# Kernel tuning notes

Hardware: AMD Instinct MI355X
Metric: run time of the kernel (lower is better)

Reference implementation:

```python
import jax, jax.numpy as jnp
import numpy as np

NBINS = 256       # kornia equalize_clahe default histogram bins
GRID = (8, 8)     # kornia default grid_size


def _clahe(x, clip_limit):
    """kornia-style CLAHE on x:(C,H,W) in [0,1]; H,W divisible by GRID."""
    C, H, W = x.shape
    GH, GW = GRID
    TH, TW = H // GH, W // GW
    pixels = TH * TW
    # ---- per-tile histograms via flat scatter-add (irregular core) ----
    b_hist = jnp.clip((x * NBINS).astype(jnp.int32), 0, NBINS - 1)  # torch.histc(min=0,max=1) bins
    tiles = b_hist.reshape(C, GH, TH, GW, TW).transpose(0, 1, 3, 2, 4).reshape(-1, pixels)
    ntiles = tiles.shape[0]  # C*GH*GW
    flat = (tiles + (jnp.arange(ntiles, dtype=jnp.int32) * NBINS)[:, None]).ravel()
    hist = jnp.zeros((ntiles * NBINS,), x.dtype).at[flat].add(1.0).reshape(ntiles, NBINS)
    # ---- clip and redistribute excess (kornia _compute_luts) ----
    max_val = jnp.maximum(jnp.floor(clip_limit * pixels / NBINS), 1.0)
    clipped = jnp.minimum(hist, max_val)
    excess = pixels - clipped.sum(-1)                    # (ntiles,), >= 0
    residual = jnp.mod(excess, NBINS)
    redist = (excess - residual) / NBINS
    hist = clipped + redist[:, None] + (jnp.arange(NBINS) < residual[:, None]).astype(x.dtype)
    # ---- LUT from CDF ----
    lut = jnp.floor(jnp.clip(jnp.cumsum(hist, -1) * (NBINS - 1) / pixels, 0, NBINS - 1))
    lut = lut.reshape(C, GH, GW, NBINS)
    # ---- per-pixel bilinear interpolation between 4 neighbouring tile LUTs ----
    def coords(n, T, G):
        g = (jnp.arange(n) + 0.5) / T - 0.5    # fractional tile coordinate
        lo = jnp.clip(jnp.floor(g), 0, G - 1).astype(jnp.int32)
        hi = jnp.clip(lo + 1, 0, G - 1)
        w = jnp.clip(g - jnp.floor(g), 0.0, 1.0).astype(x.dtype)
        return lo, hi, w
    y0, y1, wy = coords(H, TH, GH)
    x0, x1, wx = coords(W, TW, GW)
    b = jnp.clip(jnp.floor(x * (NBINS - 1)).astype(jnp.int32), 0, NBINS - 1)  # lookup bin
    c = jnp.arange(C)[:, None, None]
    def g(ty, tx):  # gather lut[c, ty[h], tx[w], b[c,h,w]] -> (C,H,W)
        return lut[c, ty[None, :, None], tx[None, None, :], b]
    top = g(y0, x0) * (1 - wx)[None, None, :] + g(y0, x1) * wx[None, None, :]
    bot = g(y1, x0) * (1 - wx)[None, None, :] + g(y1, x1) * wx[None, None, :]
    out = top * (1 - wy)[None, :, None] + bot * wy[None, :, None]
    return out / (NBINS - 1)


def _forward(x, log_cor=True):
    shape = x.shape
    mean = x.mean()
    std = jnp.std(x, ddof=1)            # torch .std() is unbiased
    x = (x - mean) / std                # TF.normalize
    xmin, xmax = x.min(), x.max()
    x = (x - xmin) / (xmax - xmin)      # normalize_in_range(x, 0, 1)
    ct_proxy = jnp.std(x, ddof=1)       # x.std([0,1,2]) on 3D input = scalar
    def clahe_branch(xx):
        beta = 10.0 * ct_proxy
        cl = 1.0 / (1.0 - beta) + beta  # data-dependent clip limit
        return _clahe(xx, cl)
    x = jax.lax.cond(ct_proxy < 0.05, clahe_branch, lambda xx: xx, x)
    if log_cor:
        x = jnp.log2(1.0 + x)           # adjust_log with gain=1
    return x.reshape(shape)


def setup_inputs() -> dict:
    key = jax.random.key(0)
    x = jax.random.normal(key, (32, 1024, 1024), dtype=jnp.float32)
    # heavy-tailed distribution -> std/range (ct_proxy) ~ 0.01 < 0.05 so CLAHE branch runs
    x = x ** 3
    return {"x": x}


def reference(x):
    return _forward(x, log_cor=True)
```

## Files before the change

### kernel.cpp

```cpp
#include <hip/hip_runtime.h>
#include <math.h>

#define NC 32
#define NH 1024
#define NW 1024
#define NGH 8
#define NGW 8
#define NTH 128
#define NTW 128
#define NBINS 256
#define NTILES (NC*NGH*NGW)
#define NPIXTOT (NC*NH*NW)
#define TPIX (NTH*NTW)

#define OFF_PSUM   0
#define OFF_PSQ    16384
#define OFF_PMIN   32768
#define OFF_PMAX   40960
#define OFF_PARAMS 49152
#define OFF_HIST   65536
#define OFF_LUT    (OFF_HIST + NTILES*NBINS*4)

__global__ __launch_bounds__(256) void k_reduce(const float* __restrict__ x,
                                                double* __restrict__ ps,
                                                double* __restrict__ ps2,
                                                float* __restrict__ pmn,
                                                float* __restrict__ pmx) {
    int tid = threadIdx.x;
    long g = (long)blockIdx.x * 256 + tid;
    double s = 0.0, s2 = 0.0;
    float mn = INFINITY, mx = -INFINITY;
    const float4* x4 = (const float4*)x;
    const long n4 = NPIXTOT / 4;
    for (long i = g; i < n4; i += (long)2048 * 256) {
        float4 v = x4[i];
        float sf  = (v.x + v.y) + (v.z + v.w);
        float s2f = fmaf(v.x, v.x, fmaf(v.y, v.y, fmaf(v.z, v.z, v.w * v.w)));
        s  += (double)sf;
        s2 += (double)s2f;
        mn = fminf(mn, fminf(fminf(v.x, v.y), fminf(v.z, v.w)));
        mx = fmaxf(mx, fmaxf(fmaxf(v.x, v.y), fmaxf(v.z, v.w)));
    }
    for (int o = 32; o; o >>= 1) {
        s  += __shfl_down(s, o);
        s2 += __shfl_down(s2, o);
        mn = fminf(mn, __shfl_down(mn, o));
        mx = fmaxf(mx, __shfl_down(mx, o));
    }
    __shared__ double shs[4], shs2[4];
    __shared__ float shmn[4], shmx[4];
    int wid = tid >> 6, lane = tid & 63;
    if (lane == 0) { shs[wid] = s; shs2[wid] = s2; shmn[wid] = mn; shmx[wid] = mx; }
    __syncthreads();
    if (tid == 0) {
        double S  = shs[0] + shs[1] + shs[2] + shs[3];
        double S2 = shs2[0] + shs2[1] + shs2[2] + shs2[3];
        float MN = fminf(fminf(shmn[0], shmn[1]), fminf(shmn[2], shmn[3]));
        float MX = fmaxf(fmaxf(shmx[0], shmx[1]), fmaxf(shmx[2], shmx[3]));
        ps[blockIdx.x] = S; ps2[blockIdx.x] = S2; pmn[blockIdx.x] = MN; pmx[blockIdx.x] = MX;
    }
}

__global__ __launch_bounds__(256) void k_params(const double* __restrict__ ps,
                                                const double* __restrict__ ps2,
                                                const float* __restrict__ pmn,
                                                const float* __restrict__ pmx,
                                                float* __restrict__ params) {
    int tid = threadIdx.x;
    double s = 0.0, s2 = 0.0;
    float mn = INFINITY, mx = -INFINITY;
    for (int i = tid; i < 2048; i += 256) {
        s += ps[i]; s2 += ps2[i];
        mn = fminf(mn, pmn[i]); mx = fmaxf(mx, pmx[i]);
    }
    for (int o = 32; o; o >>= 1) {
        s  += __shfl_down(s, o);
        s2 += __shfl_down(s2, o);
        mn = fminf(mn, __shfl_down(mn, o));
        mx = fmaxf(mx, __shfl_down(mx, o));
    }
    __shared__ double shs[4], shs2[4];
    __shared__ float shmn[4], shmx[4];
    int wid = tid >> 6, lane = tid & 63;
    if (lane == 0) { shs[wid] = s; shs2[wid] = s2; shmn[wid] = mn; shmx[wid] = mx; }
    __syncthreads();
    if (tid == 0) {
        double S  = shs[0] + shs[1] + shs[2] + shs[3];
        double S2 = shs2[0] + shs2[1] + shs2[2] + shs2[3];
        float MN = fminf(fminf(shmn[0], shmn[1]), fminf(shmn[2], shmn[3]));
        float MX = fmaxf(fmaxf(shmx[0], shmx[1]), fmaxf(shmx[2], shmx[3]));
        const double n = (double)NPIXTOT;
        double var = (S2 - S * S / n) / (n - 1.0);
        double sd = sqrt(var > 0.0 ? var : 0.0);
        double range = (double)MX - (double)MN;
        double ct = sd / range;
        int flag = (ct < 0.05) ? 1 : 0;
        double beta = 10.0 * ct;
        double cl = 1.0 / (1.0 - beta) + beta;
        double mv = floor(cl * (double)TPIX / (double)NBINS);
        if (mv < 1.0) mv = 1.0;
        params[0] = MN;
        params[1] = (float)(1.0 / range);
        params[2] = (float)mv;
        ((int*)params)[3] = flag;
    }
}

__global__ __launch_bounds__(256) void k_hist(const float* __restrict__ x,
                                              const float* __restrict__ params,
                                              unsigned* __restrict__ hist) {
    __shared__ unsigned lh[NBINS];
    int tid = threadIdx.x;
    int t = blockIdx.x;
    int lane = tid & 63;
    lh[tid] = 0;
    __syncthreads();
    float xmin = params[0], inv = params[1];
    int c = t >> 6, gy = (t >> 3) & 7, gx = t & 7;
    const float* base = x + ((long)c * NH + (long)gy * NTH) * NW + gx * NTW;
    #pragma unroll
    for (int j = 0; j < 16; j++) {
        int l = j * 256 + tid;
        int th = l >> 5, tw4 = l & 31;
        float4 v = *(const float4*)(base + (long)th * NW + tw4 * 4);
        float zv[4] = {v.x, v.y, v.z, v.w};
        #pragma unroll
        for (int k = 0; k < 4; k++) {
            float z = (zv[k] - xmin) * inv;
            int b = (int)(z * 256.0f);
            b = b < 0 ? 0 : (b > 255 ? 255 : b);
            unsigned long long alive = __ballot(1);
            #pragma unroll
            for (int r = 0; r < 3; r++) {
                if (!alive) break;
                int leader = (int)(__ffsll((long long)alive) - 1);
                int lb = __shfl(b, leader);
                unsigned long long m = __ballot(b == lb) & alive;
                if (lane == leader) atomicAdd(&lh[lb], (unsigned)__popcll(m));
                alive &= ~m;
            }
            if ((alive >> lane) & 1ull) atomicAdd(&lh[b], 1u);
        }
    }
    __syncthreads();
    hist[t * NBINS + tid] = lh[tid];
}

__global__ __launch_bounds__(256) void k_lut(const unsigned* __restrict__ hist,
                                             const float* __restrict__ params,
                                             float* __restrict__ lut) {
    int tid = threadIdx.x;
    int t = blockIdx.x;
    int mv = (int)params[2];
    int h = (int)hist[t * NBINS + tid];
    int cl = h < mv ? h : mv;
    __shared__ int sh[NBINS];
    sh[tid] = cl;
    __syncthreads();
    for (int o = 1; o < NBINS; o <<= 1) {
        int v = (tid >= o) ? sh[tid - o] : 0;
        __syncthreads();
        sh[tid] += v;
        __syncthreads();
    }
    int total = sh[NBINS - 1];
    int cdfc = sh[tid];
    int excess = TPIX - total;
    int residual = excess & (NBINS - 1);
    int redist = excess >> 8;
    int cdf = cdfc + redist * (tid + 1) + ((tid + 1) < residual ? (tid + 1) : residual);
    float lv = floorf(fminf((float)cdf * 255.0f / 16384.0f, 255.0f));
    lut[t * NBINS + tid] = lv < 0.0f ? 0.0f : lv;
}

__global__ __launch_bounds__(256) void k_out(const float* __restrict__ x,
                                             const float* __restrict__ params,
                                             const float* __restrict__ lut,
                                             float* __restrict__ out) {
    int tid = threadIdx.x;
    long fid = (long)blockIdx.x * 256 + tid;
    long p = fid * 4;
    int w = (int)(p & (NW - 1));
    int h = (int)((p >> 10) & (NH - 1));
    int c = (int)(p >> 20);
    float xmin = params[0], inv = params[1];
    int flag = ((const int*)params)[3];
    float4 v = *(const float4*)(x + p);
    float gy = (h + 0.5f) * (1.0f / NTH) - 0.5f;
    float fy = floorf(gy);
    float wy = gy - fy;
    int y0 = (int)fy; y0 = y0 < 0 ? 0 : (y0 > 7 ? 7 : y0);
    int y1 = y0 + 1 > 7 ? 7 : y0 + 1;
    const float* lutc = lut + (long)c * 64 * NBINS;
    float zv[4] = {v.x, v.y, v.z, v.w};
    float o4[4];
    #pragma unroll
    for (int k = 0; k < 4; k++) {
        float z = (zv[k] - xmin) * inv;
        float val;
        if (flag) {
            int wk = w + k;
            float gx = (wk + 0.5f) * (1.0f / NTW) - 0.5f;
            float fx = floorf(gx);
            float wx = gx - fx;
            int x0 = (int)fx; x0 = x0 < 0 ? 0 : (x0 > 7 ? 7 : x0);
            int x1 = x0 + 1 > 7 ? 7 : x0 + 1;
            int b = (int)(z * 255.0f);
            b = b < 0 ? 0 : (b > 255 ? 255 : b);
            const float* l00 = lutc + (y0 * 8 + x0) * NBINS;
            const float* l01 = lutc + (y0 * 8 + x1) * NBINS;
            const float* l10 = lutc + (y1 * 8 + x0) * NBINS;
            const float* l11 = lutc + (y1 * 8 + x1) * NBINS;
            float top = l00[b] * (1.0f - wx) + l01[b] * wx;
            float bot = l10[b] * (1.0f - wx) + l11[b] * wx;
            val = (top * (1.0f - wy) + bot * wy) * (1.0f / 255.0f);
        } else {
            val = z;
        }
        o4[k] = log2f(1.0f + val);
    }
    *(float4*)(out + p) = make_float4(o4[0], o4[1], o4[2], o4[3]);
}

extern "C" void kernel_launch(void* const* d_in, const int* in_sizes, int n_in,
                              void* d_out, int out_size, void* d_ws, size_t ws_size,
                              hipStream_t stream) {
    const float* x = (const float*)d_in[0];
    float* out = (float*)d_out;
    char* ws = (char*)d_ws;
    double* ps   = (double*)(ws + OFF_PSUM);
    double* ps2  = (double*)(ws + OFF_PSQ);
    float* pmn   = (float*)(ws + OFF_PMIN);
    float* pmx   = (float*)(ws + OFF_PMAX);
    float* params= (float*)(ws + OFF_PARAMS);
    unsigned* hist = (unsigned*)(ws + OFF_HIST);
    float* lut   = (float*)(ws + OFF_LUT);

    k_reduce<<<2048, 256, 0, stream>>>(x, ps, ps2, pmn, pmx);
    k_params<<<1, 256, 0, stream>>>(ps, ps2, pmn, pmx, params);
    k_hist<<<NTILES, 256, 0, stream>>>(x, params, hist);
    k_lut<<<NTILES, 256, 0, stream>>>(hist, params, lut);
    k_out<<<NPIXTOT / 1024, 256, 0, stream>>>(x, params, lut, out);
}
```

Baseline: 325.2 us.

## Fuse histogram and LUT kernels, use byte LUTs staged in shared memory

Merges the histogram and LUT-building kernels into one, so the intermediate histogram no longer makes a global round trip and one launch is dropped. Each wavefront now keeps its own shared-memory histogram copy to reduce atomic contention. LUT values are stored as bytes. The output kernel processes one image row per block and stages the two needed rows of tile LUTs (4 KB) in shared memory, so the bilinear gathers hit LDS instead of global memory. This adds a barrier and a LUT staging load per block, and changes how the output work is mapped to blocks.

```diff
diff --git a/kernel.cpp b/kernel.cpp
--- a/kernel.cpp
+++ b/kernel.cpp
@@ -4,12 +4,10 @@
 #define NC 32
 #define NH 1024
 #define NW 1024
-#define NGH 8
-#define NGW 8
 #define NTH 128
 #define NTW 128
 #define NBINS 256
-#define NTILES (NC*NGH*NGW)
+#define NTILES (NC*8*8)
 #define NPIXTOT (NC*NH*NW)
 #define TPIX (NTH*NTW)
 
@@ -18,8 +16,7 @@
 #define OFF_PMIN   32768
 #define OFF_PMAX   40960
 #define OFF_PARAMS 49152
-#define OFF_HIST   65536
-#define OFF_LUT    (OFF_HIST + NTILES*NBINS*4)
+#define OFF_LUT8   65536
 
 __global__ __launch_bounds__(256) void k_reduce(const float* __restrict__ x,
                                                 double* __restrict__ ps,
@@ -106,19 +103,23 @@
     }
 }
 
-__global__ __launch_bounds__(256) void k_hist(const float* __restrict__ x,
-                                              const float* __restrict__ params,
-                                              unsigned* __restrict__ hist) {
-    __shared__ unsigned lh[NBINS];
+__global__ __launch_bounds__(256) void k_histlut(const float* __restrict__ x,
+                                                 const float* __restrict__ params,
+                                                 unsigned char* __restrict__ lut8) {
+    __shared__ unsigned lh[4 * NBINS];
+    __shared__ int sh[NBINS];
     int tid = threadIdx.x;
     int t = blockIdx.x;
     int lane = tid & 63;
-    lh[tid] = 0;
+    int wid = tid >> 6;
+    #pragma unroll
+    for (int w = 0; w < 4; w++) lh[w * NBINS + tid] = 0;
     __syncthreads();
     float xmin = params[0], inv = params[1];
     int c = t >> 6, gy = (t >> 3) & 7, gx = t & 7;
     const float* base = x + ((long)c * NH + (long)gy * NTH) * NW + gx * NTW;
-    #pragma unroll
+    unsigned* mylh = lh + wid * NBINS;
+    #pragma unroll 4
     for (int j = 0; j < 16; j++) {
         int l = j * 256 + tid;
         int th = l >> 5, tw4 = l & 31;
@@ -136,25 +137,16 @@
                 int leader = (int)(__ffsll((long long)alive) - 1);
                 int lb = __shfl(b, leader);
                 unsigned long long m = __ballot(b == lb) & alive;
-                if (lane == leader) atomicAdd(&lh[lb], (unsigned)__popcll(m));
+                if (lane == leader) atomicAdd(&mylh[lb], (unsigned)__popcll(m));
                 alive &= ~m;
             }
-            if ((alive >> lane) & 1ull) atomicAdd(&lh[b], 1u);
+            if ((alive >> lane) & 1ull) atomicAdd(&mylh[b], 1u);
         }
     }
     __syncthreads();
-    hist[t * NBINS + tid] = lh[tid];
-}
-
-__global__ __launch_bounds__(256) void k_lut(const unsigned* __restrict__ hist,
-                                             const float* __restrict__ params,
-                                             float* __restrict__ lut) {
-    int tid = threadIdx.x;
-    int t = blockIdx.x;
     int mv = (int)params[2];
-    int h = (int)hist[t * NBINS + tid];
+    int h = (int)(lh[tid] + lh[NBINS + tid] + lh[2 * NBINS + tid] + lh[3 * NBINS + tid]);
     int cl = h < mv ? h : mv;
-    __shared__ int sh[NBINS];
     sh[tid] = cl;
     __syncthreads();
     for (int o = 1; o < NBINS; o <<= 1) {
@@ -170,28 +162,37 @@
     int redist = excess >> 8;
     int cdf = cdfc + redist * (tid + 1) + ((tid + 1) < residual ? (tid + 1) : residual);
     float lv = floorf(fminf((float)cdf * 255.0f / 16384.0f, 255.0f));
-    lut[t * NBINS + tid] = lv < 0.0f ? 0.0f : lv;
+    int iv = (int)(lv < 0.0f ? 0.0f : lv);
+    lut8[t * NBINS + tid] = (unsigned char)iv;
 }
 
 __global__ __launch_bounds__(256) void k_out(const float* __restrict__ x,
                                              const float* __restrict__ params,
-                                             const float* __restrict__ lut,
+                                             const unsigned char* __restrict__ lut8,
                                              float* __restrict__ out) {
-    int tid = threadIdx.x;
-    long fid = (long)blockIdx.x * 256 + tid;
-    long p = fid * 4;
-    int w = (int)(p & (NW - 1));
-    int h = (int)((p >> 10) & (NH - 1));
-    int c = (int)(p >> 20);
+    __shared__ unsigned char slut[4096];
+    int tid = threadIdx.x;
+    int r = blockIdx.x;
+    int c = r >> 10;
+    int h = r & (NH - 1);
     float xmin = params[0], inv = params[1];
     int flag = ((const int*)params)[3];
-    float4 v = *(const float4*)(x + p);
     float gy = (h + 0.5f) * (1.0f / NTH) - 0.5f;
     float fy = floorf(gy);
     float wy = gy - fy;
     int y0 = (int)fy; y0 = y0 < 0 ? 0 : (y0 > 7 ? 7 : y0);
     int y1 = y0 + 1 > 7 ? 7 : y0 + 1;
-    const float* lutc = lut + (long)c * 64 * NBINS;
+    const unsigned char* src0 = lut8 + ((long)c * 64 + y0 * 8) * NBINS;
+    const unsigned char* src1 = lut8 + ((long)c * 64 + y1 * 8) * NBINS;
+    if (tid < 128) {
+        *(uint4*)(slut + tid * 16) = *(const uint4*)(src0 + tid * 16);
+    } else {
+        int u = tid - 128;
+        *(uint4*)(slut + 2048 + u * 16) = *(const uint4*)(src1 + u * 16);
+    }
+    __syncthreads();
+    long p = ((long)r << 10) + tid * 4;
+    float4 v = *(const float4*)(x + p);
     float zv[4] = {v.x, v.y, v.z, v.w};
     float o4[4];
     #pragma unroll
@@ -199,20 +200,20 @@
         float z = (zv[k] - xmin) * inv;
         float val;
         if (flag) {
-            int wk = w + k;
-            float gx = (wk + 0.5f) * (1.0f / NTW) - 0.5f;
-            float fx = floorf(gx);
-            float wx = gx - fx;
+            int wk = tid * 4 + k;
+            float gxc = (wk + 0.5f) * (1.0f / NTW) - 0.5f;
+            float fx = floorf(gxc);
+            float wx = gxc - fx;
             int x0 = (int)fx; x0 = x0 < 0 ? 0 : (x0 > 7 ? 7 : x0);
             int x1 = x0 + 1 > 7 ? 7 : x0 + 1;
             int b = (int)(z * 255.0f);
             b = b < 0 ? 0 : (b > 255 ? 255 : b);
-            const float* l00 = lutc + (y0 * 8 + x0) * NBINS;
-            const float* l01 = lutc + (y0 * 8 + x1) * NBINS;
-            const float* l10 = lutc + (y1 * 8 + x0) * NBINS;
-            const float* l11 = lutc + (y1 * 8 + x1) * NBINS;
-            float top = l00[b] * (1.0f - wx) + l01[b] * wx;
-            float bot = l10[b] * (1.0f - wx) + l11[b] * wx;
+            float l00 = (float)slut[x0 * NBINS + b];
+            float l01 = (float)slut[x1 * NBINS + b];
+            float l10 = (float)slut[2048 + x0 * NBINS + b];
+            float l11 = (float)slut[2048 + x1 * NBINS + b];
+            float top = l00 * (1.0f - wx) + l01 * wx;
+            float bot = l10 * (1.0f - wx) + l11 * wx;
             val = (top * (1.0f - wy) + bot * wy) * (1.0f / 255.0f);
         } else {
             val = z;
@@ -233,12 +234,10 @@
     float* pmn   = (float*)(ws + OFF_PMIN);
     float* pmx   = (float*)(ws + OFF_PMAX);
     float* params= (float*)(ws + OFF_PARAMS);
-    unsigned* hist = (unsigned*)(ws + OFF_HIST);
-    float* lut   = (float*)(ws + OFF_LUT);
+    unsigned char* lut8 = (unsigned char*)(ws + OFF_LUT8);
 
     k_reduce<<<2048, 256, 0, stream>>>(x, ps, ps2, pmn, pmx);
     k_params<<<1, 256, 0, stream>>>(ps, ps2, pmn, pmx, params);
-    k_hist<<<NTILES, 256, 0, stream>>>(x, params, hist);
-    k_lut<<<NTILES, 256, 0, stream>>>(hist, params, lut);
-    k_out<<<NPIXTOT / 1024, 256, 0, stream>>>(x, params, lut, out);
-}
+    k_histlut<<<NTILES, 256, 0, stream>>>(x, params, lut8);
+    k_out<<<NC * NH, 256, 0, stream>>>(x, params, lut8, out);
+}
```

New measurement: 297.8 us. 1.09x faster.
